# Kernel tuning notes

Hardware: AMD Instinct MI355X
Metric: run time of the kernel (lower is better)

## Reference

```python
import jax, jax.numpy as jnp
import numpy as np

K = 20
EPS = 1e-5
NEG_SLOPE = 0.2


def _knn_idx(x, k):
    # x: (B, N, C). Torch: pd = -||xi||^2 + 2 xi.xj - ||xj||^2, topk largest = nearest.
    inner = jnp.einsum('bnc,bmc->bnm', x, x)
    xx = jnp.sum(x * x, axis=-1)  # (B, N)
    pd = 2.0 * inner - xx[:, :, None] - xx[:, None, :]
    _, idx = jax.lax.top_k(pd, k)  # (B, N, k)
    return idx


def _bn_lrelu(h, gamma, beta, axes):
    mean = jnp.mean(h, axis=axes)
    var = jnp.var(h, axis=axes)  # biased, as in torch BN training normalization
    hn = (h - mean) * jax.lax.rsqrt(var + EPS) * gamma + beta
    return jnp.where(hn >= 0, hn, NEG_SLOPE * hn)


def _edge_conv(x, W, gamma, beta, k):
    # x: (B, N, C); W: (O, 2C). Returns (B, N, O).
    idx = _knn_idx(x, k)
    nbr = jax.vmap(lambda xb, ib: xb[ib])(x, idx)  # (B, N, k, C) gather
    center = jnp.broadcast_to(x[:, :, None, :], nbr.shape)
    edge = jnp.concatenate([nbr - center, center], axis=-1)  # (B, N, k, 2C)
    h = jnp.einsum('bnkc,oc->bnko', edge, W)
    h = _bn_lrelu(h, gamma, beta, axes=(0, 1, 2))
    return jnp.max(h, axis=2)  # max over k -> (B, N, O)


def setup_inputs() -> dict:
    key = jax.random.key(0)
    ks = jax.random.split(key, 16)
    B, N = 32, 1024
    d = {'x': jax.random.normal(ks[0], (B, N, 3), dtype=jnp.float32)}
    dims = [(64, 6), (64, 128), (128, 128), (256, 256), (1024, 512)]
    for i, (o, c) in enumerate(dims, start=1):
        d[f'W{i}'] = jax.random.normal(ks[i], (o, c), dtype=jnp.float32) * 0.05
        d[f'g{i}'] = jnp.ones((o,), dtype=jnp.float32)
        d[f'b{i}'] = jnp.zeros((o,), dtype=jnp.float32)
    return d


def reference(x, W1, g1, b1, W2, g2, b2, W3, g3, b3, W4, g4, b4, W5, g5, b5):
    B = x.shape[0]
    x1 = _edge_conv(x, W1, g1, b1, K)    # (B, N, 64)
    x2 = _edge_conv(x1, W2, g2, b2, K)   # (B, N, 64)
    x3 = _edge_conv(x2, W3, g3, b3, K)   # (B, N, 128)
    x4 = _edge_conv(x3, W4, g4, b4, K)   # (B, N, 256)
    cat = jnp.concatenate([x1, x2, x3, x4], axis=-1)  # (B, N, 512)
    h = jnp.einsum('bnc,oc->bno', cat, W5)            # (B, N, 1024)
    h = _bn_lrelu(h, g5, b5, axes=(0, 1))
    out = jnp.max(h, axis=1)  # adaptive max pool over points -> (B, 1024)
    return out.reshape(B, 1, -1)
```

## Files before the change

### kernel.cpp

```cpp
#include <hip/hip_runtime.h>
#include <math.h>

#define BB 32
#define NN 1024
#define KNNK 20
#define PTS (BB*NN)

typedef __attribute__((ext_vector_type(8)))  short short8;
typedef __attribute__((ext_vector_type(4)))  float f32x4;
typedef __attribute__((ext_vector_type(16))) float f32x16;

__device__ __forceinline__ float lrelu(float v){ return v >= 0.f ? v : 0.2f*v; }

__device__ __forceinline__ unsigned short f2b(float x){
    union { float f; unsigned u; } c; c.f = x;
    unsigned r = c.u + 0x7FFFu + ((c.u >> 16) & 1u);
    return (unsigned short)(r >> 16);
}

__global__ void sq_kernel(const float* __restrict__ x, int stride, int C, float* __restrict__ xx){
    int pn = blockIdx.x*256 + threadIdx.x;
    if (pn >= PTS) return;
    const float* r = x + (size_t)pn*stride;
    float s = 0.f;
    if ((C & 3) == 0){
        for (int c = 0; c < C; c += 4){
            float4 v = *(const float4*)&r[c];
            s = fmaf(v.x, v.x, s); s = fmaf(v.y, v.y, s);
            s = fmaf(v.z, v.z, s); s = fmaf(v.w, v.w, s);
        }
    } else {
        for (int c = 0; c < C; ++c){ float v = r[c]; s = fmaf(v, v, s); }
    }
    xx[pn] = s;
}

template<int C>
__global__ void __launch_bounds__(512, 4) knn_kernel(const float* __restrict__ x, int stride,
                                                     const float* __restrict__ xx,
                                                     int* __restrict__ idxout){
    constexpr int KC = 8;
    __shared__ __align__(16) float Bs[2][NN][4];
    __shared__ float xs[NN];
    int bid = (int)blockIdx.x;
    bid = (bid & 7)*128 + (bid >> 3);
    const int b  = bid >> 5;
    const int rb = bid & 31;
    const int r0 = rb * 32;
    const int tid = threadIdx.x;
    const int wv = tid >> 6, lane = tid & 63;
    const float* xb = x + (size_t)b*NN*stride;

    if (tid < 256) *(float4*)&xs[tid*4] = *(const float4*)&xx[b*NN + tid*4];

    float acc[4][16];
    #pragma unroll
    for (int r=0;r<4;++r)
        #pragma unroll
        for (int q=0;q<16;++q) acc[r][q] = 0.f;

    const int wrow = wv*4;

    #pragma unroll 1
    for (int kc = 0; kc < C; kc += KC){
        __syncthreads();
        #pragma unroll
        for (int ps = 0; ps < 4; ++ps){
            int i = tid + ps*512;
            int col = i >> 1, half = i & 1;
            float4 v;
            if constexpr (C == 3){
                float vv[4];
                #pragma unroll
                for (int j = 0; j < 4; ++j){
                    int k = half*4 + j;
                    vv[j] = (k < 3) ? xb[(size_t)col*3 + k] : 0.f;
                }
                v = make_float4(vv[0], vv[1], vv[2], vv[3]);
            } else {
                v = *(const float4*)&xb[(size_t)col*stride + kc + half*4];
            }
            *(float4*)&Bs[half][col][0] = v;
        }
        __syncthreads();
        #pragma unroll
        for (int s = 0; s < 2; ++s){
            float4 ar[4];
            #pragma unroll
            for (int r=0;r<4;++r)
                ar[r] = *(const float4*)&Bs[s][r0 + wrow + r][0];
            #pragma unroll
            for (int q=0;q<16;++q){
                float4 bv = *(const float4*)&Bs[s][lane + 64*q][0];
                #pragma unroll
                for (int r=0;r<4;++r){
                    acc[r][q] = fmaf(ar[r].x, bv.x, acc[r][q]);
                    acc[r][q] = fmaf(ar[r].y, bv.y, acc[r][q]);
                    acc[r][q] = fmaf(ar[r].z, bv.z, acc[r][q]);
                    acc[r][q] = fmaf(ar[r].w, bv.w, acc[r][q]);
                }
            }
        }
    }

    const unsigned long long lt = (lane == 0) ? 0ull : ((~0ull) >> (64 - lane));
    #pragma unroll
    for (int r = 0; r < 4; ++r){
        const int lrow = r0 + wrow + r;
        const float xi = xs[lrow];
        unsigned u[16];
        #pragma unroll
        for (int q = 0; q < 16; ++q){
            float d = 2.f*acc[r][q] - xi - xs[lane + 64*q];
            unsigned bits = __float_as_uint(d);
            unsigned m = (bits & 0x80000000u) ? 0xFFFFFFFFu : 0x80000000u;
            u[q] = bits ^ m;
        }
        unsigned t = 0u;
        for (int bb = 31; bb >= 0; --bb){
            unsigned cand = t | (1u << bb);
            int cnt = 0;
            #pragma unroll
            for (int q = 0; q < 16; ++q)
                cnt += (int)__popcll(__ballot(u[q] >= cand));
            if (cnt >= KNNK) t = cand;
        }
        int* orow = idxout + ((size_t)b*NN + lrow) * KNNK;
        int cbase = 0;
        #pragma unroll
        for (int q = 0; q < 16; ++q){
            bool gt2 = (u[q] > t);
            unsigned long long mask = __ballot(gt2);
            if (gt2) orow[cbase + (int)__popcll(mask & lt)] = q*64 + lane;
            cbase += (int)__popcll(mask);
        }
        #pragma unroll
        for (int q = 0; q < 16; ++q){
            bool eq = (u[q] == t);
            unsigned long long mask = __ballot(eq);
            int pos = cbase + (int)__popcll(mask & lt);
            if (eq && pos < KNNK) orow[pos] = q*64 + lane;
            cbase += (int)__popcll(mask);
        }
    }
}

template<int C, int O>
__global__ void __launch_bounds__(256) gemmG_kernel(const float* __restrict__ x, int stride,
                                                    const float* __restrict__ W,
                                                    float* __restrict__ G1, float* __restrict__ Gd){
    constexpr int KC = (C < 32 ? C : 32);
    __shared__ float Xl [KC][68];
    __shared__ float W1l[KC][68];
    __shared__ float W2l[KC][68];
    const int tid = threadIdx.x;
    const int r0 = blockIdx.x * 64;
    const int o0 = blockIdx.y * 64;
    const int rt = tid & 15, ct = tid >> 4;

    float a1[4][4] = {{0.f}}, a2[4][4] = {{0.f}};
    for (int kc = 0; kc < C; kc += KC){
        __syncthreads();
        for (int i = tid; i < KC*64; i += 256){
            int k = i % KC, rr = i / KC;
            Xl [k][rr] = x[(size_t)(r0+rr)*stride + kc + k];
            W1l[k][rr] = W[(size_t)(o0+rr)*(2*C) + kc + k];
            W2l[k][rr] = W[(size_t)(o0+rr)*(2*C) + C + kc + k];
        }
        __syncthreads();
        #pragma unroll
        for (int k = 0; k < KC; ++k){
            float4 xa = *(const float4*)&Xl [k][rt*4];
            float4 w1 = *(const float4*)&W1l[k][ct*4];
            float4 w2 = *(const float4*)&W2l[k][ct*4];
            float xv[4] = {xa.x, xa.y, xa.z, xa.w};
            #pragma unroll
            for (int i = 0; i < 4; ++i){
                a1[i][0] = fmaf(xv[i], w1.x, a1[i][0]);
                a1[i][1] = fmaf(xv[i], w1.y, a1[i][1]);
                a1[i][2] = fmaf(xv[i], w1.z, a1[i][2]);
                a1[i][3] = fmaf(xv[i], w1.w, a1[i][3]);
                a2[i][0] = fmaf(xv[i], w2.x, a2[i][0]);
                a2[i][1] = fmaf(xv[i], w2.y, a2[i][1]);
                a2[i][2] = fmaf(xv[i], w2.z, a2[i][2]);
                a2[i][3] = fmaf(xv[i], w2.w, a2[i][3]);
            }
        }
    }
    #pragma unroll
    for (int i = 0; i < 4; ++i){
        size_t row = (size_t)(r0 + rt*4 + i);
        float4 g1v = make_float4(a1[i][0], a1[i][1], a1[i][2], a1[i][3]);
        float4 gdv = make_float4(a2[i][0]-a1[i][0], a2[i][1]-a1[i][1],
                                 a2[i][2]-a1[i][2], a2[i][3]-a1[i][3]);
        *(float4*)&G1[row*O + o0 + ct*4] = g1v;
        *(float4*)&Gd[row*O + o0 + ct*4] = gdv;
    }
}

template<int O>
__global__ void __launch_bounds__(512) gatherB_kernel(const float* __restrict__ G1,
                                                      const float* __restrict__ Gd,
                                                      const int* __restrict__ idxg, int bgbase,
                                                      float* __restrict__ catslice,
                                                      float* __restrict__ stats){
    __shared__ __align__(16) float G1s[1024][36];
    __shared__ int nbs[64][KNNK];
    const int bl = blockIdx.x;
    const int cc = blockIdx.y * 32;
    const int tid = threadIdx.x;
    const size_t prow = (size_t)bl*1024;

    for (int i = tid; i < 8192; i += 512){
        int row = i >> 3, q8 = i & 7;
        float4 v = *(const float4*)&G1[(prow + row)*O + cc + q8*4];
        *(float4*)&G1s[row][q8*4] = v;
    }

    const int c4 = (tid & 7)*4;
    const int pq = tid >> 3;
    const int lane = tid & 63;
    float S1[4] = {0.f,0.f,0.f,0.f}, S2[4] = {0.f,0.f,0.f,0.f};

    for (int ps = 0; ps < 16; ++ps){
        __syncthreads();
        for (int i = tid; i < 64*KNNK; i += 512){
            int pp = i / KNNK, kk = i - (i/KNNK)*KNNK;
            nbs[pp][kk] = idxg[((size_t)bgbase + prow + ps*64 + pp)*KNNK + kk];
        }
        __syncthreads();
        const int p = ps*64 + pq;
        float4 dv = *(const float4*)&Gd[(prow + p)*O + cc + c4];
        float d[4] = {dv.x, dv.y, dv.z, dv.w};
        float mx[4] = {-INFINITY,-INFINITY,-INFINITY,-INFINITY};
        float ls[4] = {0.f,0.f,0.f,0.f}, lq[4] = {0.f,0.f,0.f,0.f};
        #pragma unroll
        for (int kk = 0; kk < KNNK; ++kk){
            int row = nbs[pq][kk];
            float4 gv = *(const float4*)&G1s[row][c4];
            float ga[4] = {gv.x, gv.y, gv.z, gv.w};
            #pragma unroll
            for (int c = 0; c < 4; ++c){
                mx[c] = fmaxf(mx[c], ga[c]);
                ls[c] += ga[c];
                lq[c] = fmaf(ga[c], ga[c], lq[c]);
            }
        }
        float4 outv;
        float* op = &outv.x;
        #pragma unroll
        for (int c = 0; c < 4; ++c){
            S1[c] += ls[c] + 20.f*d[c];
            S2[c] += lq[c] + 2.f*d[c]*ls[c] + 20.f*d[c]*d[c];
            op[c] = mx[c] + d[c];
        }
        *(float4*)&catslice[((size_t)bgbase + prow + p)*512 + cc + c4] = outv;
    }

    #pragma unroll
    for (int c = 0; c < 4; ++c){
        #pragma unroll
        for (int m = 8; m < 64; m <<= 1){
            S1[c] += __shfl_xor(S1[c], m);
            S2[c] += __shfl_xor(S2[c], m);
        }
    }
    if (lane < 8){
        int rep = ((int)blockIdx.x*8 + (int)blockIdx.y) & 63;
        #pragma unroll
        for (int c = 0; c < 4; ++c){
            atomicAdd(&stats[rep*2*O + cc + lane*4 + c],     S1[c]);
            atomicAdd(&stats[rep*2*O + O + cc + lane*4 + c], S2[c]);
        }
    }
}

__global__ void fin_kernel(const float* __restrict__ stats, int O, float cnt,
                           float* __restrict__ mean, float* __restrict__ invstd){
    int o = threadIdx.x;
    if (o >= O) return;
    float s1 = 0.f, s2 = 0.f;
    for (int r = 0; r < 64; ++r){
        s1 += stats[r*2*O + o];
        s2 += stats[r*2*O + O + o];
    }
    float m = s1 / cnt;
    float v = s2 / cnt - m*m;
    mean[o] = m;
    invstd[o] = rsqrtf(v + 1e-5f);
}

template<int O>
__global__ void apply_kernel(float* __restrict__ catslice,
                             const float* __restrict__ mean, const float* __restrict__ invstd,
                             const float* __restrict__ g, const float* __restrict__ bt){
    int i = blockIdx.x*256 + threadIdx.x;
    int pn = i / O, o = i - pn*O;
    float* p = &catslice[(size_t)pn*512 + o];
    float hn = (*p - mean[o]) * invstd[o] * g[o] + bt[o];
    *p = lrelu(hn);
}

__global__ void tob16_kernel(const float* __restrict__ src, unsigned short* __restrict__ dst, int n4){
    int i = blockIdx.x*256 + threadIdx.x;
    if (i >= n4) return;
    float4 v = *(const float4*)&src[(size_t)i*4];
    ushort4 o;
    o.x = f2b(v.x); o.y = f2b(v.y); o.z = f2b(v.z); o.w = f2b(v.w);
    *(ushort4*)&dst[(size_t)i*4] = o;
}

__global__ void __launch_bounds__(256) l5m_kernel(const unsigned short* __restrict__ Am,
                                                  const unsigned short* __restrict__ Bm,
                                                  float* __restrict__ pmax,
                                                  float* __restrict__ psum,
                                                  float* __restrict__ psq){
    __shared__ __align__(16) unsigned short As[128][64];
    __shared__ __align__(16) unsigned short Bs[128][64];
    const int tid = threadIdx.x;
    const int r0 = blockIdx.x * 128;
    const int o0 = blockIdx.y * 128;
    const int w = tid >> 6, lane = tid & 63;
    const int m32 = lane & 31, kh = lane >> 5;
    const int wm = (w & 1) * 64;
    const int wn = (w >> 1) * 64;

    f32x16 acc[2][2];
    #pragma unroll
    for (int i=0;i<2;++i)
        #pragma unroll
        for (int j=0;j<2;++j)
            #pragma unroll
            for (int r=0;r<16;++r) acc[i][j][r] = 0.f;

    for (int kc = 0; kc < 512; kc += 64){
        __syncthreads();
        #pragma unroll
        for (int t = 0; t < 4; ++t){
            int i = tid + t*256;
            int rr = i >> 3, ch = i & 7;
            int sl = ch ^ (rr & 7);
            *(uint4*)&As[rr][sl*8] = *(const uint4*)&Am[(size_t)(r0+rr)*512 + kc + ch*8];
            *(uint4*)&Bs[rr][sl*8] = *(const uint4*)&Bm[(size_t)(o0+rr)*512 + kc + ch*8];
        }
        __syncthreads();
        #pragma unroll
        for (int q = 0; q < 4; ++q){
            int lk = q*2 + kh;
            short8 a[2], bfr[2];
            #pragma unroll
            for (int mb = 0; mb < 2; ++mb){
                int rA = wm + mb*32 + m32;
                a[mb] = *(const short8*)&As[rA][(lk ^ (rA & 7))*8];
            }
            #pragma unroll
            for (int nb = 0; nb < 2; ++nb){
                int rB = wn + nb*32 + m32;
                bfr[nb] = *(const short8*)&Bs[rB][(lk ^ (rB & 7))*8];
            }
            #pragma unroll
            for (int mb = 0; mb < 2; ++mb)
                #pragma unroll
                for (int nb = 0; nb < 2; ++nb)
                    acc[mb][nb] = __builtin_amdgcn_mfma_f32_32x32x16_bf16(a[mb], bfr[nb], acc[mb][nb], 0, 0, 0);
        }
    }
    __syncthreads();
    float* red = (float*)&As[0][0];
    #pragma unroll
    for (int nb = 0; nb < 2; ++nb){
        float mx = -INFINITY, s1 = 0.f, s2 = 0.f;
        #pragma unroll
        for (int mb = 0; mb < 2; ++mb)
            #pragma unroll
            for (int r = 0; r < 16; ++r){
                float v = acc[mb][nb][r];
                mx = fmaxf(mx, v); s1 += v; s2 = fmaf(v, v, s2);
            }
        mx = fmaxf(mx, __shfl_xor(mx, 32));
        s1 += __shfl_xor(s1, 32);
        s2 += __shfl_xor(s2, 32);
        if (lane < 32){
            int col = wn + nb*32 + m32;
            float* p = red + ((size_t)(w & 1) * 128 + col) * 3;
            p[0] = mx; p[1] = s1; p[2] = s2;
        }
    }
    __syncthreads();
    if (tid < 128){
        const float* p0 = red + (size_t)tid*3;
        const float* p1 = red + (size_t)(128 + tid)*3;
        float mx = fmaxf(p0[0], p1[0]);
        float s1 = p0[1] + p1[1];
        float s2 = p0[2] + p1[2];
        size_t pi = (size_t)blockIdx.x*1024 + o0 + tid;
        pmax[pi] = mx; psum[pi] = s1; psq[pi] = s2;
    }
}

__global__ void fin5_kernel(const float* __restrict__ pmax, const float* __restrict__ psum,
                            const float* __restrict__ psq,
                            const float* __restrict__ g, const float* __restrict__ bt,
                            float* __restrict__ out){
    int o = blockIdx.x*256 + threadIdx.x;
    float s1 = 0.f, s2 = 0.f;
    for (int r = 0; r < 256; ++r){
        s1 += psum[(size_t)r*1024 + o];
        s2 += psq [(size_t)r*1024 + o];
    }
    float m  = s1 / 32768.f;
    float v  = s2 / 32768.f - m*m;
    float is = rsqrtf(v + 1e-5f);
    float gg = g[o], bb2 = bt[o];
    for (int b = 0; b < 32; ++b){
        float mx = -INFINITY;
        #pragma unroll
        for (int ns = 0; ns < 8; ++ns) mx = fmaxf(mx, pmax[((size_t)b*8 + ns)*1024 + o]);
        float hn = (mx - m) * is * gg + bb2;
        out[(size_t)b*1024 + o] = lrelu(hn);
    }
}

extern "C" void kernel_launch(void* const* d_in, const int* in_sizes, int n_in,
                              void* d_out, int out_size, void* d_ws, size_t ws_size,
                              hipStream_t stream) {
    (void)in_sizes; (void)n_in; (void)out_size;
    const float* x  = (const float*)d_in[0];
    const float* W1 = (const float*)d_in[1];  const float* g1 = (const float*)d_in[2];  const float* b1 = (const float*)d_in[3];
    const float* W2 = (const float*)d_in[4];  const float* g2 = (const float*)d_in[5];  const float* b2 = (const float*)d_in[6];
    const float* W3 = (const float*)d_in[7];  const float* g3 = (const float*)d_in[8];  const float* b3 = (const float*)d_in[9];
    const float* W4 = (const float*)d_in[10]; const float* g4 = (const float*)d_in[11]; const float* b4 = (const float*)d_in[12];
    const float* W5 = (const float*)d_in[13]; const float* g5 = (const float*)d_in[14]; const float* b5 = (const float*)d_in[15];
    float* out = (float*)d_out;

    const size_t fixedBytes = (size_t)PTS*512*4 + (size_t)PTS*KNNK*4 + (size_t)PTS*4
                            + (size_t)64*2*256*4 + 2048*4 + 3*(size_t)256*1024*4
                            + (size_t)1024*512*2;
    int CB;
    if      (ws_size >= fixedBytes + (size_t)32*NN*NN*4) CB = 32;
    else if (ws_size >= fixedBytes + (size_t)16*NN*NN*4) CB = 16;
    else                                                 CB = 8;
    const size_t Rbytes = (size_t)CB*NN*NN*4;

    char* wsp = (char*)d_ws;
    float* cat    = (float*)wsp; wsp += (size_t)PTS*512*4;
    char*  R      = wsp;         wsp += Rbytes;
    int*   idx    = (int*)  wsp; wsp += (size_t)PTS*KNNK*4;
    float* xx     = (float*)wsp; wsp += (size_t)PTS*4;
    float* stats  = (float*)wsp; wsp += (size_t)64*2*256*4;
    float* mean   = (float*)wsp; wsp += 1024*4;
    float* invstd = (float*)wsp; wsp += 1024*4;
    float* pmax   = (float*)wsp; wsp += (size_t)256*1024*4;
    float* psum   = (float*)wsp; wsp += (size_t)256*1024*4;
    float* psq    = (float*)wsp; wsp += (size_t)256*1024*4;
    unsigned short* W5b = (unsigned short*)wsp; wsp += (size_t)1024*512*2;

    float* G1    = (float*)R;
    float* GdS   = (float*)(R + (size_t)16*1024*1024);
    float* GdB   = (float*)(R + (size_t)32*1024*1024);
    unsigned short* catB = (unsigned short*)R;

    const float cntE = (float)(PTS*KNNK);
    const bool bigG = (Rbytes >= (size_t)64*1024*1024);

    sq_kernel<<<PTS/256, 256, 0, stream>>>(x, 3, 3, xx);
    knn_kernel<3><<<1024, 512, 0, stream>>>(x, 3, xx, idx);
    hipMemsetAsync(stats, 0, 64*2*256*4, stream);
    gemmG_kernel<3,64><<<dim3(512,1), 256, 0, stream>>>(x, 3, W1, G1, GdS);
    gatherB_kernel<64><<<dim3(32,2), 512, 0, stream>>>(G1, GdS, idx, 0, cat + 0, stats);
    fin_kernel<<<1, 64, 0, stream>>>(stats, 64, cntE, mean, invstd);
    apply_kernel<64><<<PTS*64/256, 256, 0, stream>>>(cat + 0, mean, invstd, g1, b1);

    sq_kernel<<<PTS/256, 256, 0, stream>>>(cat + 0, 512, 64, xx);
    knn_kernel<64><<<1024, 512, 0, stream>>>(cat + 0, 512, xx, idx);
    hipMemsetAsync(stats, 0, 64*2*256*4, stream);
    gemmG_kernel<64,64><<<dim3(512,1), 256, 0, stream>>>(cat + 0, 512, W2, G1, GdS);
    gatherB_kernel<64><<<dim3(32,2), 512, 0, stream>>>(G1, GdS, idx, 0, cat + 64, stats);
    fin_kernel<<<1, 64, 0, stream>>>(stats, 64, cntE, mean, invstd);
    apply_kernel<64><<<PTS*64/256, 256, 0, stream>>>(cat + 64, mean, invstd, g2, b2);

    sq_kernel<<<PTS/256, 256, 0, stream>>>(cat + 64, 512, 64, xx);
    knn_kernel<64><<<1024, 512, 0, stream>>>(cat + 64, 512, xx, idx);
    hipMemsetAsync(stats, 0, 64*2*256*4, stream);
    gemmG_kernel<64,128><<<dim3(512,2), 256, 0, stream>>>(cat + 64, 512, W3, G1, GdS);
    gatherB_kernel<128><<<dim3(32,4), 512, 0, stream>>>(G1, GdS, idx, 0, cat + 128, stats);
    fin_kernel<<<1, 128, 0, stream>>>(stats, 128, cntE, mean, invstd);
    apply_kernel<128><<<PTS*128/256, 256, 0, stream>>>(cat + 128, mean, invstd, g3, b3);

    sq_kernel<<<PTS/256, 256, 0, stream>>>(cat + 128, 512, 128, xx);
    knn_kernel<128><<<1024, 512, 0, stream>>>(cat + 128, 512, xx, idx);
    hipMemsetAsync(stats, 0, 64*2*256*4, stream);
    if (bigG){
        gemmG_kernel<128,256><<<dim3(512,4), 256, 0, stream>>>(cat + 128, 512, W4, G1, GdB);
        gatherB_kernel<256><<<dim3(32,8), 512, 0, stream>>>(G1, GdB, idx, 0, cat + 256, stats);
    } else {
        for (int bg = 0; bg < 4; ++bg){
            gemmG_kernel<128,256><<<dim3(128,4), 256, 0, stream>>>(cat + 128 + (size_t)bg*8192*512, 512, W4, G1, GdS);
            gatherB_kernel<256><<<dim3(8,8), 512, 0, stream>>>(G1, GdS, idx, bg*8192, cat + 256, stats);
        }
    }
    fin_kernel<<<1, 256, 0, stream>>>(stats, 256, cntE, mean, invstd);
    apply_kernel<256><<<PTS*256/256, 256, 0, stream>>>(cat + 256, mean, invstd, g4, b4);

    tob16_kernel<<<PTS*512/4/256, 256, 0, stream>>>(cat, catB, PTS*512/4);
    tob16_kernel<<<1024*512/4/256, 256, 0, stream>>>(W5, W5b, 1024*512/4);
    l5m_kernel<<<dim3(256, 8), 256, 0, stream>>>(catB, W5b, pmax, psum, psq);
    fin5_kernel<<<4, 256, 0, stream>>>(pmax, psum, psq, g5, b5, out);
}
```

Before: 1.229 ms.

## Double-buffer kNN LDS tiles with async global-to-LDS loads

Rewrites the kNN distance kernel's channel loop to double-buffer the shared-memory tile. The next 8-channel chunk is prefetched with `global_load_lds` DMA while the current chunk is computed. This removes one barrier per chunk and the register round-trip for staging. In exchange it doubles the tile's LDS footprint, which may cut how many blocks fit per CU. It also relies on the compiler inserting correct waits for the asynchronous LDS writes.

Result: no change. 1.216 ms (-1.1%).

```diff
diff --git a/kernel.cpp b/kernel.cpp
--- a/kernel.cpp
+++ b/kernel.cpp
@@ -16,6 +16,13 @@
     union { float f; unsigned u; } c; c.f = x;
     unsigned r = c.u + 0x7FFFu + ((c.u >> 16) & 1u);
     return (unsigned short)(r >> 16);
+}
+
+__device__ __forceinline__ void glds16(const float* g, float* l){
+    __builtin_amdgcn_global_load_lds(
+        (const __attribute__((address_space(1))) unsigned int*)g,
+        (__attribute__((address_space(3))) unsigned int*)l,
+        16, 0, 0);
 }
 
 __global__ void sq_kernel(const float* __restrict__ x, int stride, int C, float* __restrict__ xx){
@@ -40,7 +47,8 @@
                                                      const float* __restrict__ xx,
                                                      int* __restrict__ idxout){
     constexpr int KC = 8;
-    __shared__ __align__(16) float Bs[2][NN][4];
+    constexpr int NCH = (C + KC - 1)/KC;
+    __shared__ __align__(16) float Bs[2][2][NN][4];
     __shared__ float xs[NN];
     int bid = (int)blockIdx.x;
     bid = (bid & 7)*128 + (bid >> 3);
@@ -61,37 +69,50 @@
 
     const int wrow = wv*4;
 
-    #pragma unroll 1
-    for (int kc = 0; kc < C; kc += KC){
-        __syncthreads();
+    if constexpr (C == 3){
         #pragma unroll
         for (int ps = 0; ps < 4; ++ps){
             int i = tid + ps*512;
             int col = i >> 1, half = i & 1;
-            float4 v;
-            if constexpr (C == 3){
-                float vv[4];
-                #pragma unroll
-                for (int j = 0; j < 4; ++j){
-                    int k = half*4 + j;
-                    vv[j] = (k < 3) ? xb[(size_t)col*3 + k] : 0.f;
-                }
-                v = make_float4(vv[0], vv[1], vv[2], vv[3]);
-            } else {
-                v = *(const float4*)&xb[(size_t)col*stride + kc + half*4];
-            }
-            *(float4*)&Bs[half][col][0] = v;
-        }
-        __syncthreads();
+            float vv[4];
+            #pragma unroll
+            for (int j = 0; j < 4; ++j){
+                int k = half*4 + j;
+                vv[j] = (k < 3) ? xb[(size_t)col*3 + k] : 0.f;
+            }
+            *(float4*)&Bs[0][half][col][0] = make_float4(vv[0],vv[1],vv[2],vv[3]);
+        }
+    } else {
+        #pragma unroll
+        for (int j = 0; j < 4; ++j){
+            int m = wv*4 + j;
+            int g = m >> 4, c0 = (m & 15)*64;
+            glds16(&xb[(size_t)(c0 + lane)*stride + g*4], &Bs[0][g][c0][0]);
+        }
+    }
+
+    #pragma unroll 1
+    for (int c = 0; c < NCH; ++c){
+        const int cur = c & 1;
+        __syncthreads();
+        if (C > 8 && c + 1 < NCH){
+            const int kc1 = (c + 1)*KC;
+            #pragma unroll
+            for (int j = 0; j < 4; ++j){
+                int m = wv*4 + j;
+                int g = m >> 4, c0 = (m & 15)*64;
+                glds16(&xb[(size_t)(c0 + lane)*stride + kc1 + g*4], &Bs[cur ^ 1][g][c0][0]);
+            }
+        }
         #pragma unroll
         for (int s = 0; s < 2; ++s){
             float4 ar[4];
             #pragma unroll
             for (int r=0;r<4;++r)
-                ar[r] = *(const float4*)&Bs[s][r0 + wrow + r][0];
+                ar[r] = *(const float4*)&Bs[cur][s][r0 + wrow + r][0];
             #pragma unroll
             for (int q=0;q<16;++q){
-                float4 bv = *(const float4*)&Bs[s][lane + 64*q][0];
+                float4 bv = *(const float4*)&Bs[cur][s][lane + 64*q][0];
                 #pragma unroll
                 for (int r=0;r<4;++r){
                     acc[r][q] = fmaf(ar[r].x, bv.x, acc[r][q]);
```
